# Kernel optimization log

Hardware: AMD Instinct MI355X
Metric: run time of the kernel (lower is better)

Reference implementation:

```python
import jax, jax.numpy as jnp
import numpy as np

NUM_USERS = 100000
NUM_ITEMS = 50000
EMBED_DIM = 64
N_LAYERS = 3
NUM_EDGES = 3276800  # avg user degree 32
BATCH = 16384


def setup_inputs() -> dict:
    key = jax.random.key(0)
    k0, k1, k2, k3, k4, k5 = jax.random.split(key, 6)
    rows = jax.random.randint(k0, (NUM_EDGES,), 0, NUM_USERS, dtype=jnp.int32)
    cols = jax.random.randint(k1, (NUM_EDGES,), 0, NUM_ITEMS, dtype=jnp.int32)
    user_table = jax.random.normal(k2, (NUM_USERS, EMBED_DIM), dtype=jnp.float32) * 0.1
    item_table = jax.random.normal(k3, (NUM_ITEMS, EMBED_DIM), dtype=jnp.float32) * 0.1
    user_indices = jax.random.randint(k4, (BATCH,), 0, NUM_USERS, dtype=jnp.int32)
    item_indices = jax.random.randint(k5, (BATCH,), 0, NUM_ITEMS, dtype=jnp.int32)
    return {
        "user_table": user_table,
        "item_table": item_table,
        "rows": rows,
        "cols": cols,
        "user_indices": user_indices,
        "item_indices": item_indices,
    }


def reference(user_table, item_table, rows, cols, user_indices, item_indices):
    # D^-1 A row-normalization of the binary bipartite adjacency:
    # normalized edge value for edge (u, i) is 1 / deg(u) (0 if isolated).
    ones = jnp.ones(rows.shape, dtype=user_table.dtype)
    deg = jax.ops.segment_sum(ones, rows, num_segments=NUM_USERS)
    inv_deg = jnp.where(deg > 0, 1.0 / deg, 0.0)
    vals = inv_deg[rows]  # [E]

    u = user_table  # [U, D] (unused by propagation in the original too)
    it = item_table  # [I, D]
    for _ in range(N_LAYERS):
        # u = A @ it  (SpMM via gather + segment-sum over destination users)
        u = jax.ops.segment_sum(vals[:, None] * it[cols], rows, num_segments=NUM_USERS)
        # it = A^T @ u
        it = jax.ops.segment_sum(vals[:, None] * u[rows], cols, num_segments=NUM_ITEMS)

    scores = jnp.sum(u[user_indices] * it[item_indices], axis=-1)  # [B]
    return jax.nn.sigmoid(scores)
```

## Files before the change

### kernel.cpp

```cpp
#include <hip/hip_runtime.h>
#include <math.h>

#define NUM_USERS 100000
#define NUM_ITEMS 50000
#define EMBED     64
#define NUM_EDGES 3276800
#define BATCH     16384
#define CAP       10752
#define NBUCK     391
#define P1_EDGES  16384
#define P1_THREADS 512

typedef _Float16 half8 __attribute__((ext_vector_type(8)));

__global__ void cvt_kernel(const float* __restrict__ in, _Float16* __restrict__ out, int n8) {
    int i = blockIdx.x * 256 + threadIdx.x;
    if (i >= n8) return;
    const float4* p = (const float4*)in + 2 * i;
    float4 a = p[0], b = p[1];
    half8 o;
    o[0] = (_Float16)a.x; o[1] = (_Float16)a.y; o[2] = (_Float16)a.z; o[3] = (_Float16)a.w;
    o[4] = (_Float16)b.x; o[5] = (_Float16)b.y; o[6] = (_Float16)b.z; o[7] = (_Float16)b.w;
    ((half8*)out)[i] = o;
}

__global__ void pass1_kernel(const int* __restrict__ rows, const int* __restrict__ cols,
                             int* __restrict__ ucur, int* __restrict__ icur,
                             int* __restrict__ rec_u, int* __restrict__ rec_i) {
    __shared__ int hu[400], bu[400], lu[400];
    __shared__ int hi[400], bi[400], li[400];
    int t = threadIdx.x;
    for (int i = t; i < 400; i += P1_THREADS) { hu[i] = 0; lu[i] = 0; hi[i] = 0; li[i] = 0; }
    __syncthreads();
    long long e0 = (long long)blockIdx.x * P1_EDGES;
    for (int i = t; i < P1_EDGES; i += P1_THREADS) {
        atomicAdd(&hu[rows[e0 + i] >> 8], 1);
        atomicAdd(&hi[cols[e0 + i] >> 7], 1);
    }
    __syncthreads();
    for (int i = t; i < 400; i += P1_THREADS) {
        int v = hu[i], vr = (v + 15) & ~15;
        bu[i] = vr ? atomicAdd(&ucur[i], vr) : 0;
        v = hi[i]; vr = (v + 15) & ~15;
        bi[i] = vr ? atomicAdd(&icur[i], vr) : 0;
    }
    __syncthreads();
    for (int i = t; i < P1_EDGES; i += P1_THREADS) {
        int r = rows[e0 + i], c = cols[e0 + i];
        int b = r >> 8;
        int pos = bu[b] + atomicAdd(&lu[b], 1);
        if (pos < CAP) rec_u[b * CAP + pos] = (c << 8) | (r & 255);
        b = c >> 7;
        pos = bi[b] + atomicAdd(&li[b], 1);
        if (pos < CAP) rec_i[b * CAP + pos] = (r << 7) | (c & 127);
    }
    __syncthreads();
    for (int i = t; i < 400; i += P1_THREADS) {
        int v = hu[i], vr = (v + 15) & ~15;
        for (int j = bu[i] + v; j < bu[i] + vr; ++j)
            if (j < CAP) rec_u[i * CAP + j] = -1;
        v = hi[i]; vr = (v + 15) & ~15;
        for (int j = bi[i] + v; j < bi[i] + vr; ++j)
            if (j < CAP) rec_i[i * CAP + j] = -1;
    }
}

template <int VBITS>
__global__ void pass2_kernel(int* __restrict__ rec, const int* __restrict__ cur,
                             int* __restrict__ deg, int* __restrict__ off,
                             float* __restrict__ inv32, int ncap) {
    const int V = 1 << VBITS, M = V - 1;
    __shared__ int buf[CAP];
    __shared__ int h[256], ex[256], cnt[256], sc[256];
    int t = threadIdx.x, b = blockIdx.x;
    long long s = (long long)b * CAP;
    int n = cur[b]; if (n > CAP) n = CAP;
    for (int i = t; i < n; i += 256) buf[i] = rec[s + i];
    if (t < V) { h[t] = 0; cnt[t] = 0; }
    __syncthreads();
    for (int i = t; i < n; i += 256) {
        int r = buf[i];
        if (r != -1) atomicAdd(&h[r & M], 1);
    }
    __syncthreads();
    if (t < V) sc[t] = h[t];
    __syncthreads();
    for (int o = 1; o < V; o <<= 1) {
        int x = (t >= o && t < V) ? sc[t - o] : 0;
        __syncthreads();
        if (t < V) sc[t] += x;
        __syncthreads();
    }
    if (t < V) {
        ex[t] = sc[t] - h[t];
        int id = b * V + t;
        if (id < ncap) {
            int v = h[t];
            deg[id] = v;
            off[id] = (int)(s + ex[t]);
            if (inv32) inv32[id] = v ? 1.0f / (float)v : 0.0f;
        }
    }
    __syncthreads();
    for (int i = t; i < n; i += 256) {
        int r = buf[i];
        if (r == -1) continue;
        int k = r & M;
        int rnk = atomicAdd(&cnt[k], 1);
        rec[s + ex[k] + rnk] = (int)(((unsigned)r) >> VBITS);
    }
}

__global__ void mark_kernel(const int* __restrict__ iidx, unsigned char* __restrict__ bm) {
    int i = blockIdx.x * 256 + threadIdx.x;
    if (i < BATCH) bm[iidx[i]] = 1;
}

__global__ void compact_kernel(const unsigned char* __restrict__ bm,
                               int* __restrict__ list, int* __restrict__ cnt) {
    int i = blockIdx.x * 256 + threadIdx.x;
    if (i < NUM_ITEMS && bm[i]) {
        int p = atomicAdd(cnt, 1);
        list[p] = i;
    }
}

__global__ void gather_u(const int* __restrict__ uoff, const int* __restrict__ udeg,
                         const int* __restrict__ csr_col, const float* __restrict__ inv32,
                         const _Float16* __restrict__ it, _Float16* __restrict__ w) {
    int row = blockIdx.x * 4 + (threadIdx.x >> 6);
    if (row >= NUM_USERS) return;
    int lane = threadIdx.x & 63;
    int slot = lane >> 3;
    int h    = lane & 7;
    int start = uoff[row];
    int end = start + udeg[row];
    half8 acc = {0, 0, 0, 0, 0, 0, 0, 0};
    for (int k = start; k < end; k += 32) {
        int e1 = end - 1;
        int i0 = k + slot, i1 = i0 + 8, i2 = i0 + 16, i3 = i0 + 24;
        int c0 = csr_col[i0 < e1 ? i0 : e1];
        int c1 = csr_col[i1 < e1 ? i1 : e1];
        int c2 = csr_col[i2 < e1 ? i2 : e1];
        int c3 = csr_col[i3 < e1 ? i3 : e1];
        c0 = i0 < end ? c0 : NUM_ITEMS;
        c1 = i1 < end ? c1 : NUM_ITEMS;
        c2 = i2 < end ? c2 : NUM_ITEMS;
        c3 = i3 < end ? c3 : NUM_ITEMS;
        half8 x0 = *(const half8*)(it + (long long)c0 * EMBED + (h << 3));
        half8 x1 = *(const half8*)(it + (long long)c1 * EMBED + (h << 3));
        half8 x2 = *(const half8*)(it + (long long)c2 * EMBED + (h << 3));
        half8 x3 = *(const half8*)(it + (long long)c3 * EMBED + (h << 3));
        acc += x0; acc += x1; acc += x2; acc += x3;
    }
    float f[8];
    #pragma unroll
    for (int j = 0; j < 8; ++j) {
        f[j] = (float)acc[j];
        f[j] += __shfl_xor(f[j], 8, 64);
        f[j] += __shfl_xor(f[j], 16, 64);
        f[j] += __shfl_xor(f[j], 32, 64);
    }
    if (lane < 8) {
        float v = inv32[row];
        float v2 = v * v;
        half8 ow;
        #pragma unroll
        for (int j = 0; j < 8; ++j) ow[j] = (_Float16)(f[j] * v2);
        *(half8*)(w + (long long)row * EMBED + (lane << 3)) = ow;
    }
}

__device__ __forceinline__ void gather_it_body(int col, int lane,
                                               const int* __restrict__ ioff,
                                               const int* __restrict__ ideg,
                                               const int* __restrict__ csc_row,
                                               const _Float16* __restrict__ w,
                                               _Float16* __restrict__ it) {
    int slot = lane >> 3;
    int h    = lane & 7;
    int start = ioff[col];
    int end = start + ideg[col];
    half8 acc = {0, 0, 0, 0, 0, 0, 0, 0};
    for (int k = start; k < end; k += 32) {
        int e1 = end - 1;
        int i0 = k + slot, i1 = i0 + 8, i2 = i0 + 16, i3 = i0 + 24;
        int r0 = csc_row[i0 < e1 ? i0 : e1];
        int r1 = csc_row[i1 < e1 ? i1 : e1];
        int r2 = csc_row[i2 < e1 ? i2 : e1];
        int r3 = csc_row[i3 < e1 ? i3 : e1];
        r0 = i0 < end ? r0 : NUM_USERS;
        r1 = i1 < end ? r1 : NUM_USERS;
        r2 = i2 < end ? r2 : NUM_USERS;
        r3 = i3 < end ? r3 : NUM_USERS;
        half8 x0 = *(const half8*)(w + (long long)r0 * EMBED + (h << 3));
        half8 x1 = *(const half8*)(w + (long long)r1 * EMBED + (h << 3));
        half8 x2 = *(const half8*)(w + (long long)r2 * EMBED + (h << 3));
        half8 x3 = *(const half8*)(w + (long long)r3 * EMBED + (h << 3));
        acc += x0; acc += x1; acc += x2; acc += x3;
    }
    float f[8];
    #pragma unroll
    for (int j = 0; j < 8; ++j) {
        f[j] = (float)acc[j];
        f[j] += __shfl_xor(f[j], 8, 64);
        f[j] += __shfl_xor(f[j], 16, 64);
        f[j] += __shfl_xor(f[j], 32, 64);
    }
    if (lane < 8) {
        half8 o;
        #pragma unroll
        for (int j = 0; j < 8; ++j) o[j] = (_Float16)f[j];
        *(half8*)(it + (long long)col * EMBED + (lane << 3)) = o;
    }
}

__global__ void gather_it(const int* __restrict__ ioff, const int* __restrict__ ideg,
                          const int* __restrict__ csc_row,
                          const _Float16* __restrict__ w, _Float16* __restrict__ it) {
    int col = blockIdx.x * 4 + (threadIdx.x >> 6);
    if (col >= NUM_ITEMS) return;
    gather_it_body(col, threadIdx.x & 63, ioff, ideg, csc_row, w, it);
}

__global__ void gather_it_list(const int* __restrict__ ioff, const int* __restrict__ ideg,
                               const int* __restrict__ csc_row,
                               const _Float16* __restrict__ w, _Float16* __restrict__ it,
                               const int* __restrict__ list, const int* __restrict__ cnt) {
    int idx = blockIdx.x * 4 + (threadIdx.x >> 6);
    if (idx >= *cnt) return;
    gather_it_body(list[idx], threadIdx.x & 63, ioff, ideg, csc_row, w, it);
}

__global__ void score_kernel(const _Float16* __restrict__ w, const _Float16* __restrict__ it,
                             const int* __restrict__ udeg,
                             const int* __restrict__ uidx, const int* __restrict__ iidx,
                             float* __restrict__ out) {
    int wave_in_block = threadIdx.x >> 6;
    int lane = threadIdx.x & 63;
    int b = blockIdx.x * 4 + wave_in_block;
    if (b >= BATCH) return;
    int ui = uidx[b];
    int ii = iidx[b];
    float s = (float)w[(long long)ui * EMBED + lane] * (float)it[(long long)ii * EMBED + lane];
    #pragma unroll
    for (int off = 32; off > 0; off >>= 1)
        s += __shfl_down(s, off, 64);
    if (lane == 0) {
        s *= (float)udeg[ui];
        out[b] = 1.0f / (1.0f + expf(-s));
    }
}

extern "C" void kernel_launch(void* const* d_in, const int* in_sizes, int n_in,
                              void* d_out, int out_size, void* d_ws, size_t ws_size,
                              hipStream_t stream) {
    const float* item_table = (const float*)d_in[1];
    const int*   rows       = (const int*)d_in[2];
    const int*   cols       = (const int*)d_in[3];
    const int*   uidx       = (const int*)d_in[4];
    const int*   iidx       = (const int*)d_in[5];
    float* out = (float*)d_out;

    char* base = (char*)d_ws;
    int*   udeg  = (int*)(base + 0);
    int*   ideg  = (int*)(base +   400000);
    int*   uoff  = (int*)(base +   600000);
    int*   ioff  = (int*)(base +  1000000);
    float* inv32 = (float*)(base + 1200000);
    int*   ucur  = (int*)(base +  1600000);
    int*   icur  = (int*)(base +  1601600);
    int*   lcnt  = (int*)(base +  1603200);
    int*   ilist = (int*)(base +  1603264);
    unsigned char* bm = (unsigned char*)(base + 1668800);
    int*   rec_u = (int*)(base +  1720320);
    int*   rec_i = (int*)(base + 18923520);
    _Float16* w16  = (_Float16*)(base + 36126720);
    _Float16* it16 = (_Float16*)(base + 48926848);

    (void)hipMemsetAsync(base + 1600000, 0, 3204, stream);
    (void)hipMemsetAsync(bm, 0, NUM_ITEMS, stream);
    (void)hipMemsetAsync(w16 + (long long)NUM_USERS * EMBED, 0, 128, stream);
    (void)hipMemsetAsync(it16 + (long long)NUM_ITEMS * EMBED, 0, 128, stream);

    cvt_kernel<<<(NUM_ITEMS * EMBED / 8 + 255) / 256, 256, 0, stream>>>(
        item_table, it16, NUM_ITEMS * EMBED / 8);

    pass1_kernel<<<NUM_EDGES / P1_EDGES, P1_THREADS, 0, stream>>>(
        rows, cols, ucur, icur, rec_u, rec_i);
    pass2_kernel<8><<<NBUCK, 256, 0, stream>>>(rec_u, ucur, udeg, uoff, inv32, NUM_USERS);
    pass2_kernel<7><<<NBUCK, 256, 0, stream>>>(rec_i, icur, ideg, ioff, (float*)nullptr, NUM_ITEMS);

    mark_kernel<<<BATCH / 256, 256, 0, stream>>>(iidx, bm);
    compact_kernel<<<(NUM_ITEMS + 255) / 256, 256, 0, stream>>>(bm, ilist, lcnt);

    const int ublocks = (NUM_USERS + 3) / 4;
    const int iblocks = (NUM_ITEMS + 3) / 4;
    for (int l = 0; l < 3; ++l) {
        gather_u<<<ublocks, 256, 0, stream>>>(uoff, udeg, rec_u, inv32, it16, w16);
        if (l < 2)
            gather_it<<<iblocks, 256, 0, stream>>>(ioff, ideg, rec_i, w16, it16);
        else
            gather_it_list<<<BATCH / 4, 256, 0, stream>>>(ioff, ideg, rec_i, w16, it16,
                                                          ilist, lcnt);
    }

    score_kernel<<<BATCH / 4, 256, 0, stream>>>(w16, it16, udeg, uidx, iidx, out);
}
```

Before: 475.5 us.

## Stage bucketed records in LDS for coalesced writes; unroll item gather to 8

The bucketing pass now sorts each block's edges into per-bucket runs in shared memory using prefix scans. It then writes them to global memory as contiguous int4 stores with -1 padding, replacing scattered per-edge global writes and a serial padding loop. Separately, the item gather loop processes 64 edges per iteration with 8 independent loads per lane instead of 4, to raise memory-level parallelism. The trade-off is a 64KB shared buffer that limits pass1 occupancy, plus extra barriers for the scans and higher register use in the gather.

```diff
diff --git a/kernel.cpp b/kernel.cpp
--- a/kernel.cpp
+++ b/kernel.cpp
@@ -24,13 +24,16 @@
     ((half8*)out)[i] = o;
 }
 
-__global__ void pass1_kernel(const int* __restrict__ rows, const int* __restrict__ cols,
-                             int* __restrict__ ucur, int* __restrict__ icur,
-                             int* __restrict__ rec_u, int* __restrict__ rec_i) {
-    __shared__ int hu[400], bu[400], lu[400];
-    __shared__ int hi[400], bi[400], li[400];
+__global__ void __launch_bounds__(P1_THREADS)
+pass1_kernel(const int* __restrict__ rows, const int* __restrict__ cols,
+             int* __restrict__ ucur, int* __restrict__ icur,
+             int* __restrict__ rec_u, int* __restrict__ rec_i) {
+    __shared__ int hu[400], hi[400], gu[400], gi[400];
+    __shared__ int lbase[400], lcur[400];
+    __shared__ int sc[512];
+    __shared__ int recbuf[P1_EDGES];
     int t = threadIdx.x;
-    for (int i = t; i < 400; i += P1_THREADS) { hu[i] = 0; lu[i] = 0; hi[i] = 0; li[i] = 0; }
+    for (int i = t; i < 400; i += P1_THREADS) { hu[i] = 0; hi[i] = 0; }
     __syncthreads();
     long long e0 = (long long)blockIdx.x * P1_EDGES;
     for (int i = t; i < P1_EDGES; i += P1_THREADS) {
@@ -39,29 +42,100 @@
     }
     __syncthreads();
     for (int i = t; i < 400; i += P1_THREADS) {
-        int v = hu[i], vr = (v + 15) & ~15;
-        bu[i] = vr ? atomicAdd(&ucur[i], vr) : 0;
-        v = hi[i]; vr = (v + 15) & ~15;
-        bi[i] = vr ? atomicAdd(&icur[i], vr) : 0;
-    }
+        int vr = (hu[i] + 15) & ~15;
+        gu[i] = vr ? atomicAdd(&ucur[i], vr) : 0;
+        vr = (hi[i] + 15) & ~15;
+        gi[i] = vr ? atomicAdd(&icur[i], vr) : 0;
+    }
+
+    __syncthreads();
+    sc[t] = (t < 400) ? hu[t] : 0;
+    __syncthreads();
+    for (int o = 1; o < 512; o <<= 1) {
+        int x = (t >= o) ? sc[t - o] : 0; __syncthreads();
+        sc[t] += x; __syncthreads();
+    }
+    if (t < 400) { lbase[t] = sc[t] - hu[t]; lcur[t] = 0; }
     __syncthreads();
     for (int i = t; i < P1_EDGES; i += P1_THREADS) {
         int r = rows[e0 + i], c = cols[e0 + i];
         int b = r >> 8;
-        int pos = bu[b] + atomicAdd(&lu[b], 1);
-        if (pos < CAP) rec_u[b * CAP + pos] = (c << 8) | (r & 255);
-        b = c >> 7;
-        pos = bi[b] + atomicAdd(&li[b], 1);
-        if (pos < CAP) rec_i[b * CAP + pos] = (r << 7) | (c & 127);
-    }
-    __syncthreads();
-    for (int i = t; i < 400; i += P1_THREADS) {
-        int v = hu[i], vr = (v + 15) & ~15;
-        for (int j = bu[i] + v; j < bu[i] + vr; ++j)
-            if (j < CAP) rec_u[i * CAP + j] = -1;
-        v = hi[i]; vr = (v + 15) & ~15;
-        for (int j = bi[i] + v; j < bi[i] + vr; ++j)
-            if (j < CAP) rec_i[i * CAP + j] = -1;
+        int p = lbase[b] + atomicAdd(&lcur[b], 1);
+        recbuf[p] = (c << 8) | (r & 255);
+    }
+    __syncthreads();
+    sc[t] = (t < 400) ? ((hu[t] + 15) & ~15) : 0;
+    __syncthreads();
+    for (int o = 1; o < 512; o <<= 1) {
+        int x = (t >= o) ? sc[t - o] : 0; __syncthreads();
+        sc[t] += x; __syncthreads();
+    }
+    int total = sc[511];
+    for (int o4 = t * 4; o4 < total; o4 += P1_THREADS * 4) {
+        int lo = 0, hi_ = 399;
+        while (lo < hi_) { int mid = (lo + hi_) >> 1; if (sc[mid] > o4) hi_ = mid; else lo = mid + 1; }
+        int b = lo;
+        int v = hu[b];
+        int vr = (v + 15) & ~15;
+        int j = o4 - (sc[b] - vr);
+        int gpos = gu[b] + j;
+        if (gpos + 3 < CAP) {
+            int4 val;
+            val.x = (j + 0 < v) ? recbuf[lbase[b] + j + 0] : -1;
+            val.y = (j + 1 < v) ? recbuf[lbase[b] + j + 1] : -1;
+            val.z = (j + 2 < v) ? recbuf[lbase[b] + j + 2] : -1;
+            val.w = (j + 3 < v) ? recbuf[lbase[b] + j + 3] : -1;
+            *(int4*)(rec_u + (long long)b * CAP + gpos) = val;
+        } else {
+            for (int k = 0; k < 4; ++k)
+                if (gpos + k < CAP)
+                    rec_u[(long long)b * CAP + gpos + k] = (j + k < v) ? recbuf[lbase[b] + j + k] : -1;
+        }
+    }
+
+    __syncthreads();
+    sc[t] = (t < 400) ? hi[t] : 0;
+    __syncthreads();
+    for (int o = 1; o < 512; o <<= 1) {
+        int x = (t >= o) ? sc[t - o] : 0; __syncthreads();
+        sc[t] += x; __syncthreads();
+    }
+    if (t < 400) { lbase[t] = sc[t] - hi[t]; lcur[t] = 0; }
+    __syncthreads();
+    for (int i = t; i < P1_EDGES; i += P1_THREADS) {
+        int r = rows[e0 + i], c = cols[e0 + i];
+        int b = c >> 7;
+        int p = lbase[b] + atomicAdd(&lcur[b], 1);
+        recbuf[p] = (r << 7) | (c & 127);
+    }
+    __syncthreads();
+    sc[t] = (t < 400) ? ((hi[t] + 15) & ~15) : 0;
+    __syncthreads();
+    for (int o = 1; o < 512; o <<= 1) {
+        int x = (t >= o) ? sc[t - o] : 0; __syncthreads();
+        sc[t] += x; __syncthreads();
+    }
+    total = sc[511];
+    for (int o4 = t * 4; o4 < total; o4 += P1_THREADS * 4) {
+        int lo = 0, hi_ = 399;
+        while (lo < hi_) { int mid = (lo + hi_) >> 1; if (sc[mid] > o4) hi_ = mid; else lo = mid + 1; }
+        int b = lo;
+        int v = hi[b];
+        int vr = (v + 15) & ~15;
+        int j = o4 - (sc[b] - vr);
+        int gpos = gi[b] + j;
+        if (gpos + 3 < CAP) {
+            int4 val;
+            val.x = (j + 0 < v) ? recbuf[lbase[b] + j + 0] : -1;
+            val.y = (j + 1 < v) ? recbuf[lbase[b] + j + 1] : -1;
+            val.z = (j + 2 < v) ? recbuf[lbase[b] + j + 2] : -1;
+            val.w = (j + 3 < v) ? recbuf[lbase[b] + j + 3] : -1;
+            *(int4*)(rec_i + (long long)b * CAP + gpos) = val;
+        } else {
+            for (int k = 0; k < 4; ++k)
+                if (gpos + k < CAP)
+                    rec_i[(long long)b * CAP + gpos + k] = (j + k < v) ? recbuf[lbase[b] + j + k] : -1;
+        }
     }
 }
 
@@ -182,22 +256,22 @@
     int start = ioff[col];
     int end = start + ideg[col];
     half8 acc = {0, 0, 0, 0, 0, 0, 0, 0};
-    for (int k = start; k < end; k += 32) {
+    for (int k = start; k < end; k += 64) {
         int e1 = end - 1;
-        int i0 = k + slot, i1 = i0 + 8, i2 = i0 + 16, i3 = i0 + 24;
-        int r0 = csc_row[i0 < e1 ? i0 : e1];
-        int r1 = csc_row[i1 < e1 ? i1 : e1];
-        int r2 = csc_row[i2 < e1 ? i2 : e1];
-        int r3 = csc_row[i3 < e1 ? i3 : e1];
-        r0 = i0 < end ? r0 : NUM_USERS;
-        r1 = i1 < end ? r1 : NUM_USERS;
-        r2 = i2 < end ? r2 : NUM_USERS;
-        r3 = i3 < end ? r3 : NUM_USERS;
-        half8 x0 = *(const half8*)(w + (long long)r0 * EMBED + (h << 3));
-        half8 x1 = *(const half8*)(w + (long long)r1 * EMBED + (h << 3));
-        half8 x2 = *(const half8*)(w + (long long)r2 * EMBED + (h << 3));
-        half8 x3 = *(const half8*)(w + (long long)r3 * EMBED + (h << 3));
-        acc += x0; acc += x1; acc += x2; acc += x3;
+        int idx[8], r[8];
+        #pragma unroll
+        for (int q = 0; q < 8; ++q) {
+            idx[q] = k + slot + q * 8;
+            int safe = idx[q] < e1 ? idx[q] : e1;
+            r[q] = csc_row[safe];
+            r[q] = idx[q] < end ? r[q] : NUM_USERS;
+        }
+        half8 x[8];
+        #pragma unroll
+        for (int q = 0; q < 8; ++q)
+            x[q] = *(const half8*)(w + (long long)r[q] * EMBED + (h << 3));
+        #pragma unroll
+        for (int q = 0; q < 8; ++q) acc += x[q];
     }
     float f[8];
     #pragma unroll
```

Result: no change. 477.4 us (+0.4%).
